# Kernel tuning notes

Measured on AMD Instinct MI355X. Metric: run time of the kernel, lower is better.

The kernel has to match this reference:

```python
import jax, jax.numpy as jnp
import numpy as np


def setup_inputs() -> dict:
    key = jax.random.key(0)
    k1, k2, k3 = jax.random.split(key, 3)
    d_in, d_sae, N = 2048, 16384, 8192
    x = jax.random.normal(k1, (N, d_in), dtype=jnp.float32)
    W_enc = jax.random.normal(k2, (d_in, d_sae), dtype=jnp.float32) * (1.0 / np.sqrt(d_in))
    W_dec = jax.random.normal(k3, (d_sae, d_in), dtype=jnp.float32)
    # normalize decoder rows (SAE convention; check_decoder_norms expects unit rows)
    W_dec = W_dec / jnp.linalg.norm(W_dec, axis=1, keepdims=True)
    b_enc = jnp.zeros((d_sae,), dtype=jnp.float32)
    b_dec = jnp.zeros((d_in,), dtype=jnp.float32)
    return {"x": x, "W_enc": W_enc, "W_dec": W_dec, "b_enc": b_enc, "b_dec": b_dec, "k": 64}


def reference(x, W_enc, W_dec, b_enc, b_dec, k):
    # encode: dense matmul then top-k masking with ReLU on kept activations
    pre_acts = x @ W_enc + b_enc                      # [N, d_sae]
    top_acts, top_idx = jax.lax.top_k(pre_acts, k)    # [N, k] each
    N = pre_acts.shape[0]
    rows = jnp.arange(N)[:, None]                     # [N, 1]
    acts = jnp.zeros_like(pre_acts).at[rows, top_idx].set(jax.nn.relu(top_acts))
    # decode
    recon = acts @ W_dec + b_dec                      # [N, d_in]
    return recon
```

## Files before the change

### kernel.cpp

```cpp
#include <hip/hip_runtime.h>

#define M_ROWS 8192
#define K_DIM  2048
#define N_SAE  16384
#define TOPK   64
#define WEPS   0.027f

typedef __attribute__((ext_vector_type(8))) short bf16x8;
typedef __attribute__((ext_vector_type(4))) float f32x4;

__device__ __forceinline__ unsigned short f2bf(float f) {
  unsigned u = __float_as_uint(f);
  u += 0x7FFFu + ((u >> 16) & 1u);
  return (unsigned short)(u >> 16);
}

__device__ __forceinline__ float key2float(unsigned k) {
  unsigned short bits = (k & 0x8000u) ? (unsigned short)(k ^ 0x8000u)
                                      : (unsigned short)(~k);
  _Float16 h;
  __builtin_memcpy(&h, &bits, 2);
  return (float)h;
}

__device__ __forceinline__ void gload16(const void* g, void* l) {
  __builtin_amdgcn_global_load_lds(
      (const __attribute__((address_space(1))) unsigned int*)g,
      (__attribute__((address_space(3))) unsigned int*)l, 16, 0, 0);
}

__global__ __launch_bounds__(256) void k_convx(const float* __restrict__ x,
                                               unsigned short* __restrict__ xb) {
  const long i = ((long)blockIdx.x * 256 + threadIdx.x) * 4;
  float4 v = *(const float4*)(x + i);
  ushort4 o;
  o.x = f2bf(v.x); o.y = f2bf(v.y); o.z = f2bf(v.z); o.w = f2bf(v.w);
  *(ushort4*)(xb + i) = o;
}

__global__ __launch_bounds__(256) void k_transpose(const float* __restrict__ W,
                                                   float* __restrict__ Wt,
                                                   unsigned short* __restrict__ Wtb) {
  __shared__ float tile[32][33];
  const int nb = blockIdx.x * 32;
  const int kb = blockIdx.y * 32;
  const int tx = threadIdx.x & 31;
  const int ty = threadIdx.x >> 5;
#pragma unroll
  for (int i = 0; i < 32; i += 8)
    tile[ty + i][tx] = W[(long)(kb + ty + i) * N_SAE + nb + tx];
  __syncthreads();
#pragma unroll
  for (int i = 0; i < 32; i += 8) {
    float v = tile[tx][ty + i];
    long o = (long)(nb + ty + i) * K_DIM + kb + tx;
    Wt[o] = v;
    Wtb[o] = f2bf(v);
  }
}

__global__ __launch_bounds__(512, 2) void k_gemm(const unsigned short* __restrict__ A,
                                                 const unsigned short* __restrict__ B,
                                                 const float* __restrict__ b_enc,
                                                 _Float16* __restrict__ C) {
  __shared__ unsigned short lds[4 * 16384];
  const int t = threadIdx.x;
  const int lane = t & 63;
  const int w = t >> 6;
  const int wm = w >> 2, wn = w & 3;
  const int ml = lane & 15, kh = lane >> 4;

  const int bid = blockIdx.x;
  const int swz = (bid & 7) * 256 + (bid >> 3);
  const int bn = (swz & 63) * 256;
  const int bm = (swz >> 6) * 256;

  const int r0 = t >> 2;
  const int c0 = (t & 3) ^ (r0 & 3) ^ ((r0 >> 2) & 3);
  const int r1 = r0 + 128;
  const int c1 = (t & 3) ^ (r1 & 3) ^ ((r1 >> 2) & 3);
  const unsigned short* gA0 = A + (long)(bm + r0) * K_DIM + c0 * 8;
  const unsigned short* gA1 = A + (long)(bm + r1) * K_DIM + c1 * 8;
  const unsigned short* gB0 = B + (long)(bn + r0) * K_DIM + c0 * 8;
  const unsigned short* gB1 = B + (long)(bn + r1) * K_DIM + c1 * 8;
  char* lb = (char*)lds;
  const int dA0 = t * 16,          dA1 = 8192 + t * 16;
  const int dB0 = 16384 + t * 16,  dB1 = 24576 + t * 16;

  const int fx = (ml & 3) ^ ((ml >> 2) & 3);
  const int offA0 = (wm * 128 + ml) * 64 + ((kh ^ fx) * 16);
  const int offB0 = 16384 + (wn * 64 + ml) * 64 + ((kh ^ fx) * 16);

  f32x4 acc[8][4] = {};

#define STAGE(kt_) do {                         \
    const int bb_ = ((kt_) & 3) * 32768;        \
    const int ko_ = (kt_) * 32;                 \
    gload16(gA0 + ko_, lb + bb_ + dA0);         \
    gload16(gA1 + ko_, lb + bb_ + dA1);         \
    gload16(gB0 + ko_, lb + bb_ + dB0);         \
    gload16(gB1 + ko_, lb + bb_ + dB1);         \
  } while (0)

  STAGE(0);
  asm volatile("" ::: "memory");
  STAGE(1);
  asm volatile("" ::: "memory");
  STAGE(2);

  for (int kt = 0; kt < 64; ++kt) {
    if (kt < 62)       asm volatile("s_waitcnt vmcnt(8)" ::: "memory");
    else if (kt == 62) asm volatile("s_waitcnt vmcnt(4)" ::: "memory");
    else               asm volatile("s_waitcnt vmcnt(0)" ::: "memory");
    __builtin_amdgcn_s_barrier();
    asm volatile("" ::: "memory");
    if (kt < 61) STAGE(kt + 3);
    const char* bp = lb + (kt & 3) * 32768;
    bf16x8 af[8], bv[4];
#pragma unroll
    for (int mi = 0; mi < 8; ++mi) af[mi] = *(const bf16x8*)(bp + offA0 + mi * 1024);
#pragma unroll
    for (int ni = 0; ni < 4; ++ni) bv[ni] = *(const bf16x8*)(bp + offB0 + ni * 1024);
    __builtin_amdgcn_s_setprio(1);
#pragma unroll
    for (int mi = 0; mi < 8; ++mi)
#pragma unroll
      for (int ni = 0; ni < 4; ++ni)
        acc[mi][ni] = __builtin_amdgcn_mfma_f32_16x16x32_bf16(af[mi], bv[ni], acc[mi][ni], 0, 0, 0);
    __builtin_amdgcn_s_setprio(0);
  }
#undef STAGE

#pragma unroll
  for (int ni = 0; ni < 4; ++ni) {
    const int gn = bn + wn * 64 + ni * 16 + ml;
    const float bias = b_enc[gn];
#pragma unroll
    for (int mi = 0; mi < 8; ++mi) {
      const int gm0 = bm + wm * 128 + mi * 16 + kh * 4;
#pragma unroll
      for (int rr = 0; rr < 4; ++rr)
        C[(long)(gm0 + rr) * N_SAE + gn] = (_Float16)(acc[mi][ni][rr] + bias);
    }
  }
}

__global__ __launch_bounds__(256) void k_select(const unsigned short* __restrict__ pre,
                                                int* __restrict__ def_idx,
                                                int* __restrict__ amb_idx,
                                                int* __restrict__ counts) {
  __shared__ unsigned short keys[16384];
  __shared__ unsigned int hist[256];
  __shared__ unsigned int scan[256];
  __shared__ unsigned int sc[8];
  const long row = blockIdx.x;
  const int t = threadIdx.x;
  const uint4* src = (const uint4*)(pre + row * N_SAE);
  uint4* kdst = (uint4*)keys;
#pragma unroll
  for (int i = 0; i < 8; i++) {
    uint4 v = src[i * 256 + t];
    uint4 o;
    unsigned s;
    s = v.x & 0x80008000u; o.x = v.x ^ (0x80008000u | ((s >> 15) * 0x7FFFu));
    s = v.y & 0x80008000u; o.y = v.y ^ (0x80008000u | ((s >> 15) * 0x7FFFu));
    s = v.z & 0x80008000u; o.z = v.z ^ (0x80008000u | ((s >> 15) * 0x7FFFu));
    s = v.w & 0x80008000u; o.w = v.w ^ (0x80008000u | ((s >> 15) * 0x7FFFu));
    kdst[i * 256 + t] = o;
  }
  hist[t] = 0;
  if (t < 8) sc[t] = 0;
  __syncthreads();
  for (int i = 0; i < 64; i++) {
    unsigned k = keys[i * 256 + t];
    atomicAdd(&hist[k >> 8], 1u);
  }
  __syncthreads();
  scan[t] = hist[t];
  __syncthreads();
  for (int off = 1; off < 256; off <<= 1) {
    unsigned v = (t + off < 256) ? scan[t + off] : 0u;
    __syncthreads();
    scan[t] += v;
    __syncthreads();
  }
  if (scan[t] >= TOPK && (t == 255 || scan[t + 1] < TOPK)) {
    sc[0] = (unsigned)t;
    sc[1] = (t == 255) ? 0u : scan[t + 1];
  }
  __syncthreads();
  const unsigned bstar = sc[0];
  const unsigned H = sc[1];
  hist[t] = 0;
  __syncthreads();
  for (int i = 0; i < 64; i++) {
    unsigned k = keys[i * 256 + t];
    if ((k >> 8) == bstar) atomicAdd(&hist[k & 255u], 1u);
  }
  __syncthreads();
  scan[t] = hist[t];
  __syncthreads();
  for (int off = 1; off < 256; off <<= 1) {
    unsigned v = (t + off < 256) ? scan[t + off] : 0u;
    __syncthreads();
    scan[t] += v;
    __syncthreads();
  }
  if (H + scan[t] >= TOPK && (t == 255 || H + scan[t + 1] < TOPK)) sc[2] = (unsigned)t;
  __syncthreads();
  const unsigned T = (bstar << 8) | sc[2];
  const float tf = key2float(T);
  const float lo = tf - WEPS;
  const float hi = tf + WEPS;
  for (int i = 0; i < 64; i++) {
    unsigned k = keys[i * 256 + t];
    float vf = key2float(k);
    if (vf > hi) {
      unsigned p = atomicAdd(&sc[3], 1u);
      def_idx[row * 64 + p] = i * 256 + t;
    } else if (vf >= lo) {
      unsigned p = atomicAdd(&sc[4], 1u);
      if (p < 64) amb_idx[row * 64 + p] = i * 256 + t;
    }
  }
  __syncthreads();
  if (t == 0) {
    counts[row * 2]     = (int)sc[3];
    counts[row * 2 + 1] = (int)(sc[4] < 64u ? sc[4] : 64u);
  }
}

__global__ __launch_bounds__(256) void k_exact2(const float* __restrict__ x,
                                                const float* __restrict__ Wt,
                                                const float* __restrict__ b_enc,
                                                const _Float16* __restrict__ pre,
                                                const int* __restrict__ def_idx,
                                                const int* __restrict__ amb_idx,
                                                const int* __restrict__ counts,
                                                int* __restrict__ tidx,
                                                float* __restrict__ tact) {
  __shared__ float xs[2048];
  __shared__ double vals[64];
  __shared__ int idxs[64];
  const int row = blockIdx.x;
  const int t = threadIdx.x;
  {
    const float4* src = (const float4*)(x + (long)row * K_DIM);
    ((float4*)xs)[t] = src[t];
    ((float4*)xs)[t + 256] = src[t + 256];
  }
  const int ndef = counts[row * 2];
  const int namb = counts[row * 2 + 1];
  if (t < 64) {
    idxs[t] = (t < namb) ? amb_idx[row * 64 + t] : -1;
    vals[t] = -1e300;
  }
  __syncthreads();
  const int wave = t >> 6, lane = t & 63;
  for (int c = wave; c < namb; c += 4) {
    const int f = idxs[c];
    const float4* w = (const float4*)(Wt + (long)f * K_DIM);
    const float4* xv4 = (const float4*)xs;
    double s = 0.0;
#pragma unroll
    for (int j = 0; j < 8; j++) {
      float4 wv = w[j * 64 + lane];
      float4 xv = xv4[j * 64 + lane];
      s += (double)wv.x * (double)xv.x;
      s += (double)wv.y * (double)xv.y;
      s += (double)wv.z * (double)xv.z;
      s += (double)wv.w * (double)xv.w;
    }
#pragma unroll
    for (int off = 32; off > 0; off >>= 1) s += __shfl_down(s, off);
    if (lane == 0) vals[c] = s + (double)b_enc[f];
  }
  __syncthreads();
  for (int kk = 2; kk <= 64; kk <<= 1) {
    for (int j = kk >> 1; j > 0; j >>= 1) {
      if (t < 64) {
        const int p = t ^ j;
        if (p > t) {
          const bool up = ((t & kk) == 0);
          double a = vals[t], b = vals[p];
          if (up ? (a < b) : (a > b)) {
            vals[t] = b; vals[p] = a;
            int tmp = idxs[t]; idxs[t] = idxs[p]; idxs[p] = tmp;
          }
        }
      }
      __syncthreads();
    }
  }
  if (t < ndef) {
    const int f = def_idx[row * 64 + t];
    const float v = (float)pre[(long)row * N_SAE + f];
    tidx[row * TOPK + t] = f;
    tact[row * TOPK + t] = v > 0.f ? v : 0.f;
  }
  const int need = TOPK - ndef;
  if (t < need) {
    int f = idxs[t];
    double v = vals[t];
    if (f < 0) { f = 0; v = 0.0; }
    tidx[row * TOPK + ndef + t] = f;
    tact[row * TOPK + ndef + t] = (float)(v > 0.0 ? v : 0.0);
  }
}

__global__ __launch_bounds__(256) void k_decode(const float* __restrict__ Wd,
                                                const float* __restrict__ b_dec,
                                                const int* __restrict__ tidx,
                                                const float* __restrict__ tact,
                                                float* __restrict__ out) {
  __shared__ int fid[TOPK];
  __shared__ float fac[TOPK];
  const int row = blockIdx.x, t = threadIdx.x;
  if (t < TOPK) {
    fid[t] = tidx[row * TOPK + t];
    fac[t] = tact[row * TOPK + t];
  }
  __syncthreads();
  float4 acc0 = ((const float4*)b_dec)[t * 2];
  float4 acc1 = ((const float4*)b_dec)[t * 2 + 1];
  for (int i = 0; i < TOPK; i++) {
    const float a = fac[i];
    const float4* w = (const float4*)(Wd + (long)fid[i] * K_DIM) + t * 2;
    float4 w0 = w[0], w1 = w[1];
    acc0.x += a * w0.x; acc0.y += a * w0.y; acc0.z += a * w0.z; acc0.w += a * w0.w;
    acc1.x += a * w1.x; acc1.y += a * w1.y; acc1.z += a * w1.z; acc1.w += a * w1.w;
  }
  float4* o = (float4*)(out + (long)row * K_DIM);
  o[t * 2] = acc0;
  o[t * 2 + 1] = acc1;
}

extern "C" void kernel_launch(void* const* d_in, const int* in_sizes, int n_in,
                              void* d_out, int out_size, void* d_ws, size_t ws_size,
                              hipStream_t stream) {
  const float* x     = (const float*)d_in[0];
  const float* W_enc = (const float*)d_in[1];
  const float* W_dec = (const float*)d_in[2];
  const float* b_enc = (const float*)d_in[3];
  const float* b_dec = (const float*)d_in[4];
  float* out = (float*)d_out;
  char* ws = (char*)d_ws;

  const size_t OFF_WT   = 0;
  const size_t OFF_XB   = 134217728;
  const size_t OFF_TIDX = 134217728;
  const size_t OFF_TACT = 136314880;
  const size_t OFF_WTB  = 167772160;
  const size_t OFF_PRE  = 234881024;
  const size_t OFF_DEF  = 503316480;
  const size_t OFF_AMB  = 505413632;
  const size_t OFF_CNT  = 507510784;

  float*          WencT = (float*)(ws + OFF_WT);
  unsigned short* xb    = (unsigned short*)(ws + OFF_XB);
  unsigned short* Wtb   = (unsigned short*)(ws + OFF_WTB);
  _Float16*       pre   = (_Float16*)(ws + OFF_PRE);
  int*            didx  = (int*)(ws + OFF_DEF);
  int*            aidx  = (int*)(ws + OFF_AMB);
  int*            cnt   = (int*)(ws + OFF_CNT);
  int*            tidx  = (int*)(ws + OFF_TIDX);
  float*          tact  = (float*)(ws + OFF_TACT);

  k_convx<<<M_ROWS * K_DIM / 1024, 256, 0, stream>>>(x, xb);
  k_transpose<<<dim3(N_SAE / 32, K_DIM / 32), 256, 0, stream>>>(W_enc, WencT, Wtb);
  k_gemm<<<2048, 512, 0, stream>>>(xb, Wtb, b_enc, pre);
  k_select<<<M_ROWS, 256, 0, stream>>>((const unsigned short*)pre, didx, aidx, cnt);
  k_exact2<<<M_ROWS, 256, 0, stream>>>(x, WencT, b_enc, pre, didx, aidx, cnt, tidx, tact);
  k_decode<<<M_ROWS, 256, 0, stream>>>(W_dec, b_dec, tidx, tact, out);
}
```

Before: 1.841 ms.

## Restructure encoder GEMM into ping-pong K=64 tiles with interleaved quarter-stage loads

Replaces the 4-stage K=32 LDS ring in the encoder GEMM with two 64 KB K=64 buffers. Each tile is split into four MFMA quarters, and global loads for A/B sub-chunks are interleaved between the quarters, separated by explicit barriers, lgkmcnt/vmcnt waits and sched_barriers. It also switches to a 128-byte-row XOR swizzle. The aim is finer overlap of global-to-LDS traffic with MFMA work and fewer bank conflicts, at the cost of more barriers per K step and more fragile hand-scheduled wait counts. The tail iterations clamp the chunk index to 31 and reload already-consumed data instead of skipping those loads.

```diff
diff --git a/kernel.cpp b/kernel.cpp
--- a/kernel.cpp
+++ b/kernel.cpp
@@ -59,11 +59,24 @@
   }
 }
 
+__device__ __forceinline__ void mkchunk(int type, int u, int bm, int bn, int& g, int& l) {
+  const int kb = u & 127;
+  int row;
+  if (type == 0)      row = (u < 8192) ? (u >> 7) : (128 + ((u - 8192) >> 7));
+  else if (type == 1) row = (u < 8192) ? (64 + (u >> 7)) : (192 + ((u - 8192) >> 7));
+  else if (type == 2) row = (u >> 12) * 64 + ((u >> 7) & 31);
+  else                row = (u >> 12) * 64 + 32 + ((u >> 7) & 31);
+  l = ((type >= 2) ? 32768 : 0) + row * 128 + kb;
+  const int kbs = kb ^ ((row & 7) << 4);
+  g = ((type >= 2 ? bn : bm) + row) * K_DIM + (kbs >> 1);
+}
+
 __global__ __launch_bounds__(512, 2) void k_gemm(const unsigned short* __restrict__ A,
                                                  const unsigned short* __restrict__ B,
                                                  const float* __restrict__ b_enc,
                                                  _Float16* __restrict__ C) {
-  __shared__ unsigned short lds[4 * 16384];
+  __shared__ unsigned short lds[2 * 32768];
+  char* lb = (char*)lds;
   const int t = threadIdx.x;
   const int lane = t & 63;
   const int w = t >> 6;
@@ -75,61 +88,100 @@
   const int bn = (swz & 63) * 256;
   const int bm = (swz >> 6) * 256;
 
-  const int r0 = t >> 2;
-  const int c0 = (t & 3) ^ (r0 & 3) ^ ((r0 >> 2) & 3);
-  const int r1 = r0 + 128;
-  const int c1 = (t & 3) ^ (r1 & 3) ^ ((r1 >> 2) & 3);
-  const unsigned short* gA0 = A + (long)(bm + r0) * K_DIM + c0 * 8;
-  const unsigned short* gA1 = A + (long)(bm + r1) * K_DIM + c1 * 8;
-  const unsigned short* gB0 = B + (long)(bn + r0) * K_DIM + c0 * 8;
-  const unsigned short* gB1 = B + (long)(bn + r1) * K_DIM + c1 * 8;
-  char* lb = (char*)lds;
-  const int dA0 = t * 16,          dA1 = 8192 + t * 16;
-  const int dB0 = 16384 + t * 16,  dB1 = 24576 + t * 16;
-
-  const int fx = (ml & 3) ^ ((ml >> 2) & 3);
-  const int offA0 = (wm * 128 + ml) * 64 + ((kh ^ fx) * 16);
-  const int offB0 = 16384 + (wn * 64 + ml) * 64 + ((kh ^ fx) * 16);
+  int gA1[2], lA1[2], gA2[2], lA2[2], gB1[2], lB1[2], gB2[2], lB2[2];
+  mkchunk(0, t * 16,        bm, bn, gA1[0], lA1[0]);
+  mkchunk(0, t * 16 + 8192, bm, bn, gA1[1], lA1[1]);
+  mkchunk(1, t * 16,        bm, bn, gA2[0], lA2[0]);
+  mkchunk(1, t * 16 + 8192, bm, bn, gA2[1], lA2[1]);
+  mkchunk(2, t * 16,        bm, bn, gB1[0], lB1[0]);
+  mkchunk(2, t * 16 + 8192, bm, bn, gB1[1], lB1[1]);
+  mkchunk(3, t * 16,        bm, bn, gB2[0], lB2[0]);
+  mkchunk(3, t * 16 + 8192, bm, bn, gB2[1], lB2[1]);
+
+  const int swx = (ml & 7) << 4;
+  const int aof0 = (wm * 128 + ml) * 128 + ((kh * 16) ^ swx);
+  const int aof1 = (wm * 128 + ml) * 128 + ((64 + kh * 16) ^ swx);
+  const int bof0 = 32768 + (wn * 64 + ml) * 128 + ((kh * 16) ^ swx);
+  const int bof1 = 32768 + (wn * 64 + ml) * 128 + ((64 + kh * 16) ^ swx);
 
   f32x4 acc[8][4] = {};
-
-#define STAGE(kt_) do {                         \
-    const int bb_ = ((kt_) & 3) * 32768;        \
-    const int ko_ = (kt_) * 32;                 \
-    gload16(gA0 + ko_, lb + bb_ + dA0);         \
-    gload16(gA1 + ko_, lb + bb_ + dA1);         \
-    gload16(gB0 + ko_, lb + bb_ + dB0);         \
-    gload16(gB1 + ko_, lb + bb_ + dB1);         \
+  bf16x8 af[4][2], bv01[2][2], bv23[2][2];
+
+#define STG(P, gv, lv, bb, ktc) do {                       \
+    gload16(P + gv[0] + (ktc) * 64, lb + (bb) + lv[0]);    \
+    gload16(P + gv[1] + (ktc) * 64, lb + (bb) + lv[1]); } while (0)
+
+#define RD_A(CB, MB) do { _Pragma("unroll")                                          \
+    for (int mi = 0; mi < 4; ++mi) {                                                 \
+      af[mi][0] = *(const bf16x8*)(lb + (CB) + aof0 + ((MB) + mi) * 2048);           \
+      af[mi][1] = *(const bf16x8*)(lb + (CB) + aof1 + ((MB) + mi) * 2048); } } while (0)
+
+#define RD_B(DST, CB, NB) do { _Pragma("unroll")                                     \
+    for (int ni = 0; ni < 2; ++ni) {                                                 \
+      DST[ni][0] = *(const bf16x8*)(lb + (CB) + bof0 + ((NB) + ni) * 2048);          \
+      DST[ni][1] = *(const bf16x8*)(lb + (CB) + bof1 + ((NB) + ni) * 2048); } } while (0)
+
+#define MFMA_Q(BV, MB, NB) do {                                                      \
+    __builtin_amdgcn_s_setprio(1);                                                   \
+    _Pragma("unroll")                                                                \
+    for (int mi = 0; mi < 4; ++mi) { _Pragma("unroll")                               \
+      for (int ni = 0; ni < 2; ++ni) {                                               \
+        acc[(MB)+mi][(NB)+ni] = __builtin_amdgcn_mfma_f32_16x16x32_bf16(             \
+            af[mi][0], BV[ni][0], acc[(MB)+mi][(NB)+ni], 0, 0, 0);                   \
+        acc[(MB)+mi][(NB)+ni] = __builtin_amdgcn_mfma_f32_16x16x32_bf16(             \
+            af[mi][1], BV[ni][1], acc[(MB)+mi][(NB)+ni], 0, 0, 0);                   \
+      } }                                                                            \
+    __builtin_amdgcn_s_setprio(0); } while (0)
+
+#define SBAR  __builtin_amdgcn_sched_barrier(0)
+#define LGKM0 do { asm volatile("s_waitcnt lgkmcnt(0)" ::: "memory"); SBAR; } while (0)
+#define VMC6  do { asm volatile("s_waitcnt vmcnt(6)" ::: "memory"); SBAR; } while (0)
+#define BAR   do { __builtin_amdgcn_s_barrier(); SBAR; } while (0)
+
+#define TILE(CB, S1, S2, S3, S4) do {             \
+    RD_A(CB, 0); RD_B(bv01, CB, 0);               \
+    S1;                                           \
+    BAR; LGKM0; MFMA_Q(bv01, 0, 0); BAR;          \
+    RD_B(bv23, CB, 2);                            \
+    S2;                                           \
+    BAR; LGKM0; MFMA_Q(bv23, 0, 2); BAR;          \
+    RD_A(CB, 4);                                  \
+    S3;                                           \
+    BAR; LGKM0; MFMA_Q(bv23, 4, 2); BAR;          \
+    S4;                                           \
+    VMC6; BAR; MFMA_Q(bv01, 4, 0); BAR;           \
   } while (0)
 
-  STAGE(0);
-  asm volatile("" ::: "memory");
-  STAGE(1);
-  asm volatile("" ::: "memory");
-  STAGE(2);
-
-  for (int kt = 0; kt < 64; ++kt) {
-    if (kt < 62)       asm volatile("s_waitcnt vmcnt(8)" ::: "memory");
-    else if (kt == 62) asm volatile("s_waitcnt vmcnt(4)" ::: "memory");
-    else               asm volatile("s_waitcnt vmcnt(0)" ::: "memory");
-    __builtin_amdgcn_s_barrier();
-    asm volatile("" ::: "memory");
-    if (kt < 61) STAGE(kt + 3);
-    const char* bp = lb + (kt & 3) * 32768;
-    bf16x8 af[8], bv[4];
-#pragma unroll
-    for (int mi = 0; mi < 8; ++mi) af[mi] = *(const bf16x8*)(bp + offA0 + mi * 1024);
-#pragma unroll
-    for (int ni = 0; ni < 4; ++ni) bv[ni] = *(const bf16x8*)(bp + offB0 + ni * 1024);
-    __builtin_amdgcn_s_setprio(1);
-#pragma unroll
-    for (int mi = 0; mi < 8; ++mi)
-#pragma unroll
-      for (int ni = 0; ni < 4; ++ni)
-        acc[mi][ni] = __builtin_amdgcn_mfma_f32_16x16x32_bf16(af[mi], bv[ni], acc[mi][ni], 0, 0, 0);
-    __builtin_amdgcn_s_setprio(0);
-  }
-#undef STAGE
+  STG(A, gA1, lA1, 0, 0);
+  STG(B, gB1, lB1, 0, 0);
+  STG(B, gB2, lB2, 0, 0);
+  STG(A, gA2, lA2, 0, 0);
+  STG(A, gA1, lA1, 65536, 1);
+  STG(B, gB1, lB1, 65536, 1);
+  STG(B, gB2, lB2, 65536, 1);
+  VMC6;
+  BAR;
+
+  for (int i = 0; i < 16; ++i) {
+    const int o  = 2 * i + 1;
+    const int c2 = (2 * i + 2 < 32) ? 2 * i + 2 : 31;
+    const int c3 = (2 * i + 3 < 32) ? 2 * i + 3 : 31;
+    TILE(0,
+         STG(A, gA2, lA2, 65536, o),
+         STG(A, gA1, lA1, 0, c2),
+         STG(B, gB1, lB1, 0, c2),
+         STG(B, gB2, lB2, 0, c2));
+    TILE(65536,
+         STG(A, gA2, lA2, 0, c2),
+         STG(A, gA1, lA1, 65536, c3),
+         STG(B, gB1, lB1, 65536, c3),
+         STG(B, gB2, lB2, 65536, c3));
+  }
+#undef TILE
+#undef STG
+#undef RD_A
+#undef RD_B
+#undef MFMA_Q
 
 #pragma unroll
   for (int ni = 0; ni < 4; ++ni) {
```

New measurement: 1.760 ms. -4.4%, faster.
